# Kernel optimization log

Measured on AMD Instinct MI355X. Metric: run time of the kernel, lower is better.

Reference implementation:

```python
import jax, jax.numpy as jnp
import numpy as np
import math

H = 32          # num heads
D_NOPE = 128
D_ROPE = 64
D_QK = D_NOPE + D_ROPE   # 192
D_V = 128
KV_LORA = 512
EPS = 1e-6
ROPE_THETA = 10000.0
FACTOR = 40.0
BETA_FAST, BETA_SLOW = 32.0, 1.0
ORIG_MAX_POS = 4096
MSCALE_ALL_DIM = 1.0


def _yarn_inv_freq():
    dim = D_ROPE
    pos_freqs = ROPE_THETA ** (np.arange(0, dim, 2, dtype=np.float64) / dim)
    inv_extra = 1.0 / pos_freqs
    inv_inter = 1.0 / (FACTOR * pos_freqs)

    def corr_dim(n_rot):
        return dim * math.log(ORIG_MAX_POS / (n_rot * 2 * math.pi)) / (2 * math.log(ROPE_THETA))
    low = max(math.floor(corr_dim(BETA_FAST)), 0)
    high = min(math.ceil(corr_dim(BETA_SLOW)), dim - 1)
    ramp = np.clip((np.arange(dim // 2, dtype=np.float64) - low) / max(high - low, 1e-3), 0, 1)
    inv_freq_mask = 1.0 - ramp  # extrapolation_factor = 1
    inv_freq = inv_inter * (1 - inv_freq_mask) + inv_extra * inv_freq_mask
    return jnp.asarray(inv_freq, dtype=jnp.float32)  # [D_ROPE//2]


def _apply_rope_gptj(x, cos, sin):
    # x: [T, n, D_ROPE]; cos/sin: [T, D_ROPE//2]; interleaved (is_neox_style=False)
    x2 = x.reshape(*x.shape[:-1], D_ROPE // 2, 2)
    x1, xo = x2[..., 0], x2[..., 1]
    c = cos[:, None, :]
    s = sin[:, None, :]
    r1 = x1 * c - xo * s
    r2 = xo * c + x1 * s
    return jnp.stack([r1, r2], axis=-1).reshape(x.shape)


def _rmsnorm(x, w):
    var = jnp.mean(x.astype(jnp.float32) ** 2, axis=-1, keepdims=True)
    return (x * jax.lax.rsqrt(var + EPS)) * w


def setup_inputs() -> dict:
    key = jax.random.key(0)
    ks = jax.random.split(key, 8)
    T, HID = 2048, 4096
    def w(k, shape, fan_in):
        return jax.random.normal(k, shape, dtype=jnp.float32) * (1.0 / math.sqrt(fan_in))
    return {
        "positions": jnp.arange(T, dtype=jnp.int32),
        "hidden_states": jax.random.normal(ks[0], (T, HID), dtype=jnp.float32),
        "Wqa": w(ks[1], (HID, 1536), HID),
        "q_a_ln": jnp.ones((1536,), dtype=jnp.float32),
        "Wqb": w(ks[2], (1536, H * D_QK), 1536),
        "Wkva": w(ks[3], (HID, KV_LORA + D_ROPE), HID),
        "kv_a_ln": jnp.ones((KV_LORA,), dtype=jnp.float32),
        "Wkvb": w(ks[4], (KV_LORA, H * (D_NOPE + D_V)), KV_LORA),
        "Wo": w(ks[5], (H * D_V, HID), H * D_V),
    }


def reference(positions, hidden_states, Wqa, q_a_ln, Wqb, Wkva, kv_a_ln, Wkvb, Wo):
    T = hidden_states.shape[0]
    # softmax scaling with yarn mscale correction
    mscale = 0.1 * MSCALE_ALL_DIM * math.log(FACTOR) + 1.0
    scaling = (D_QK ** -0.5) * mscale * mscale

    # --- low-rank Q path ---
    q = hidden_states @ Wqa                       # [T, 1536]
    q = _rmsnorm(q, q_a_ln)
    q = (q @ Wqb).reshape(T, H, D_QK)             # [T, H, 192]
    q_nope, q_pe = q[..., :D_NOPE], q[..., D_NOPE:]

    # --- low-rank latent KV path ---
    latent = hidden_states @ Wkva                 # [T, 576]
    kv_a = _rmsnorm(latent[:, :KV_LORA], kv_a_ln) # [T, 512]
    k_pe = latent[:, None, KV_LORA:]              # [T, 1, 64]
    kv = (kv_a @ Wkvb).reshape(T, H, D_NOPE + D_V)
    k_nope = kv[..., :D_NOPE]                     # [T, H, 128]
    v = kv[..., D_NOPE:]                          # [T, H, 128]

    # --- decoupled RoPE on rope slice only ---
    inv_freq = _yarn_inv_freq()
    freqs = positions.astype(jnp.float32)[:, None] * inv_freq[None, :]  # [T, 32]
    cos, sin = jnp.cos(freqs), jnp.sin(freqs)
    q_pe = _apply_rope_gptj(q_pe, cos, sin)       # [T, H, 64]
    k_pe = _apply_rope_gptj(k_pe, cos, sin)       # [T, 1, 64]

    q = jnp.concatenate([q_nope, q_pe], axis=-1)                      # [T, H, 192]
    k = jnp.concatenate([k_nope, jnp.broadcast_to(k_pe, (T, H, D_ROPE))], axis=-1)

    # --- causal MHA over assembled K/V ---
    scores = jnp.einsum('thd,shd->hts', q, k) * scaling               # [H, T, T]
    causal = positions[None, :, None] >= positions[None, None, :]
    scores = jnp.where(causal, scores, jnp.finfo(scores.dtype).min)
    probs = jax.nn.softmax(scores, axis=-1)
    attn = jnp.einsum('hts,shd->thd', probs, v).reshape(T, H * D_V)
    return attn @ Wo                                                   # [T, 4096]
```

## Files before the change

### kernel.cpp

```cpp
#include <hip/hip_runtime.h>
#include <math.h>

typedef __bf16 bf16x8 __attribute__((ext_vector_type(8)));
typedef float f32x4 __attribute__((ext_vector_type(4)));
typedef unsigned short u16;
typedef unsigned int u32;

#define T_SEQ 2048
#define NHEAD 32

__device__ __forceinline__ u16 f2bu(float f){
  u32 u = __float_as_uint(f);
  u32 r = (u + 0x7fffu + ((u >> 16) & 1u)) >> 16;
  return (u16)r;
}

__device__ __forceinline__ void gload_lds16(const void* g, void* l){
  __builtin_amdgcn_global_load_lds((const __attribute__((address_space(1))) u32*)g,
                                   (__attribute__((address_space(3))) u32*)l, 16, 0, 0);
}

__global__ void cast_f32_bf16(const float* __restrict__ in, u16* __restrict__ out, int n4){
  int i = blockIdx.x * blockDim.x + threadIdx.x;
  int stride = gridDim.x * blockDim.x;
  for (; i < n4; i += stride){
    float4 v = ((const float4*)in)[i];
    ushort4 o;
    o.x = f2bu(v.x); o.y = f2bu(v.y); o.z = f2bu(v.z); o.w = f2bu(v.w);
    ((ushort4*)out)[i] = o;
  }
}

__global__ void transpose_cast(const float* __restrict__ src, u16* __restrict__ dst,
                               int K, int N){
  __shared__ float tile[64][65];
  int k0 = blockIdx.x * 64, n0 = blockIdx.y * 64;
  int t = threadIdx.x;
  int rr = t >> 4, c4 = (t & 15) * 4;
  #pragma unroll
  for (int i = 0; i < 4; i++){
    int r = rr + i * 16;
    int n = n0 + c4;
    float4 v;
    if (n < N) v = *(const float4*)(src + (size_t)(k0 + r) * N + n);
    else       v = make_float4(0.f, 0.f, 0.f, 0.f);
    tile[r][c4]     = v.x;
    tile[r][c4 + 1] = v.y;
    tile[r][c4 + 2] = v.z;
    tile[r][c4 + 3] = v.w;
  }
  __syncthreads();
  #pragma unroll
  for (int i = 0; i < 4; i++){
    int n = rr + i * 16;
    ushort4 o;
    o.x = f2bu(tile[c4 + 0][n]);
    o.y = f2bu(tile[c4 + 1][n]);
    o.z = f2bu(tile[c4 + 2][n]);
    o.w = f2bu(tile[c4 + 3][n]);
    *(ushort4*)(dst + (size_t)(n0 + n) * K + k0 + c4) = o;
  }
}

__global__ void rope_table(const int* __restrict__ positions, float* __restrict__ cosT,
                           float* __restrict__ sinT, float lo, float denom){
  int idx = blockIdx.x * blockDim.x + threadIdx.x;
  if (idx >= T_SEQ * 32) return;
  int t = idx >> 5, i = idx & 31;
  float pf = powf(10000.f, (float)i / 32.f);
  float inv_extra = 1.f / pf;
  float inv_inter = 1.f / (40.f * pf);
  float ramp = fminf(fmaxf(((float)i - lo) / denom, 0.f), 1.f);
  float invf = inv_inter * ramp + inv_extra * (1.f - ramp);
  float fr = (float)positions[t] * invf;
  cosT[idx] = cosf(fr);
  sinT[idx] = sinf(fr);
}

__global__ void rmsnorm_cast(const float* __restrict__ in, int istride, int n,
                             const float* __restrict__ w, u16* __restrict__ out, int ostride){
  int row = blockIdx.x;
  const float* x = in + (size_t)row * istride;
  float ss = 0.f;
  for (int c = threadIdx.x; c < n; c += blockDim.x){ float v = x[c]; ss += v * v; }
  #pragma unroll
  for (int off = 1; off < 64; off <<= 1) ss += __shfl_xor(ss, off);
  __shared__ float wsum[4];
  if ((threadIdx.x & 63) == 0) wsum[threadIdx.x >> 6] = ss;
  __syncthreads();
  float tot = wsum[0] + wsum[1] + wsum[2] + wsum[3];
  float scale = rsqrtf(tot / (float)n + 1e-6f);
  for (int c = threadIdx.x; c < n; c += blockDim.x)
    out[(size_t)row * ostride + c] = f2bu(x[c] * scale * w[c]);
}

__global__ void rope_kpe(const float* __restrict__ lat, int lstride, int loff,
                         const float* __restrict__ cosT,
                         const float* __restrict__ sinT, u16* __restrict__ kpe){
  int idx = blockIdx.x * blockDim.x + threadIdx.x;
  if (idx >= T_SEQ * 32) return;
  int t = idx >> 5, i = idx & 31;
  float x1 = lat[(size_t)t * lstride + loff + 2 * i];
  float x2 = lat[(size_t)t * lstride + loff + 2 * i + 1];
  float c = cosT[idx], s = sinT[idx];
  kpe[t * 64 + 2 * i]     = f2bu(x1 * c - x2 * s);
  kpe[t * 64 + 2 * i + 1] = f2bu(x2 * c + x1 * s);
}

__global__ void build_vt(const u16* __restrict__ Vtmp, u16* __restrict__ Vt){
  __shared__ u16 tile[128][72];
  int t0 = blockIdx.x * 64;
  int h = blockIdx.y;
  #pragma unroll
  for (int i = 0; i < 32; i++){
    int lin = threadIdx.x + i * 256;
    int tt = lin >> 7, dd = lin & 127;
    tile[dd][tt] = Vtmp[(size_t)(t0 + tt) * 4096 + h * 128 + dd];
  }
  __syncthreads();
  #pragma unroll
  for (int i = 0; i < 32; i++){
    int lin = threadIdx.x + i * 256;
    int dd = lin >> 6, tt = lin & 63;
    Vt[(size_t)(h * 128 + dd) * T_SEQ + t0 + tt] = tile[dd][tt];
  }
}

template<int EPI>
__global__ __launch_bounds__(256) void gemm_bt(const u16* __restrict__ A, const u16* __restrict__ BT,
                                               float* __restrict__ C, u16* __restrict__ O1,
                                               u16* __restrict__ O2,
                                               const float* __restrict__ cosT,
                                               const float* __restrict__ sinT,
                                               float scaling, int M, int N, int K){
  __shared__ __align__(1024) char lds[32768];
  const int tid = threadIdx.x;
  const int wave = tid >> 6, lane = tid & 63;
  const int lg = lane >> 4, lm = lane & 15;

  int gx = gridDim.x;
  int nwg = gx * gridDim.y;
  int orig = blockIdx.y * gx + blockIdx.x;
  int qq = nwg >> 3, rr_ = nwg & 7, xc = orig & 7, rest = orig >> 3;
  int wg = (xc < rr_ ? xc * (qq + 1) : rr_ * (qq + 1) + (xc - rr_) * qq) + rest;
  const int bn = (wg % gx) * 128, bm = (wg / gx) * 128;

  const int wr = (wave >> 1) * 64, wc = (wave & 1) * 64;
  f32x4 acc[4][4] = {};
  int srow[2], scol[2], soff[2];
  #pragma unroll
  for (int j = 0; j < 2; j++){
    int o = (wave * 2 + j) * 1024 + lane * 16;
    int row = o >> 6;
    int cg = ((o >> 4) & 3) ^ ((row >> 1) & 3);
    srow[j] = row; scol[j] = cg * 8; soff[j] = (wave * 2 + j) * 1024;
  }

  #pragma unroll
  for (int j = 0; j < 2; j++){
    gload_lds16(A  + (size_t)(bm + srow[j]) * K + scol[j], lds + soff[j]);
    gload_lds16(BT + (size_t)(bn + srow[j]) * K + scol[j], lds + 16384 + soff[j]);
  }

  int cur = 0;
  for (int k0 = 0; k0 < K; k0 += 32){
    if (k0 + 32 < K){
      char* dA = lds + (cur ^ 1) * 8192;
      char* dB = lds + 16384 + (cur ^ 1) * 8192;
      #pragma unroll
      for (int j = 0; j < 2; j++){
        gload_lds16(A  + (size_t)(bm + srow[j]) * K + k0 + 32 + scol[j], dA + soff[j]);
        gload_lds16(BT + (size_t)(bn + srow[j]) * K + k0 + 32 + scol[j], dB + soff[j]);
      }
      asm volatile("s_waitcnt vmcnt(4)" ::: "memory");
    } else {
      asm volatile("s_waitcnt vmcnt(0)" ::: "memory");
    }
    __builtin_amdgcn_sched_barrier(0);
    __builtin_amdgcn_s_barrier();

    const char* ldsA = lds + cur * 8192;
    const char* ldsB = lds + 16384 + cur * 8192;
    bf16x8 af[4], bfr[4];
    #pragma unroll
    for (int m = 0; m < 4; m++){
      int r = wr + m * 16 + lm;
      af[m] = *(const bf16x8*)(ldsA + r * 64 + ((lg ^ ((r >> 1) & 3)) << 4));
    }
    #pragma unroll
    for (int n = 0; n < 4; n++){
      int r = wc + n * 16 + lm;
      bfr[n] = *(const bf16x8*)(ldsB + r * 64 + ((lg ^ ((r >> 1) & 3)) << 4));
    }
    __builtin_amdgcn_s_setprio(1);
    #pragma unroll
    for (int m = 0; m < 4; m++)
      #pragma unroll
      for (int n = 0; n < 4; n++)
        acc[m][n] = __builtin_amdgcn_mfma_f32_16x16x32_bf16(af[m], bfr[n], acc[m][n], 0, 0, 0);
    __builtin_amdgcn_s_setprio(0);
    __builtin_amdgcn_s_barrier();
    cur ^= 1;
  }

  #pragma unroll
  for (int m = 0; m < 4; m++)
    #pragma unroll
    for (int n = 0; n < 4; n++)
      #pragma unroll
      for (int q = 0; q < 4; q++){
        int r = bm + wr + m * 16 + lg * 4 + q;
        int c = bn + wc + n * 16 + lm;
        float v = acc[m][n][q];
        if (EPI == 0){
          C[(size_t)r * N + c] = v;
        } else if (EPI == 1){
          float vp = __shfl_xor(v, 1);
          int h = c / 192, d = c - h * 192;
          float outv;
          if (d < 128) outv = v;
          else {
            int i = (d - 128) >> 1;
            float co = cosT[r * 32 + i], si = sinT[r * 32 + i];
            outv = (d & 1) ? (v * co + vp * si) : (v * co - vp * si);
          }
          O1[(size_t)h * T_SEQ * 192 + (size_t)r * 192 + d] = f2bu(outv * scaling);
        } else {
          int h = c >> 8, d = c & 255;
          if (d < 128) O1[(size_t)h * T_SEQ * 128 + (size_t)r * 128 + d] = f2bu(v);
          else         O2[(size_t)r * 4096 + h * 128 + (d - 128)] = f2bu(v);
        }
      }
}

__global__ __launch_bounds__(512, 1) void flash_attn(const u16* __restrict__ Qp, const u16* __restrict__ Kp,
                                                     const u16* __restrict__ kpe, const u16* __restrict__ Vt,
                                                     u16* __restrict__ attnb){
  const int b = blockIdx.x;
  const int h = (b & 7) + 8 * ((b >> 3) & 3);
  const int s = b >> 5;
  const int tid = threadIdx.x;
  const int wave = tid >> 6, lane = tid & 63;
  const int lg = lane >> 4, lm = lane & 15;

  __shared__ __align__(1024) char lds[141312];
  u16* Pw = (u16*)(lds + 122880 + wave * 2304);

  const u16* KpH = Kp + (size_t)h * T_SEQ * 128;
  const u16* VtH = Vt + (size_t)h * 128 * T_SEQ;

  int kO[3], kLoc[3], kPE[3];
  #pragma unroll
  for (int j = 0; j < 3; j++){
    int o = tid + 512 * j;
    int r = o / 24, c = o - r * 24;
    int cx = c ^ (r & 7);
    kO[j] = o * 16;
    if (cx < 16){ kPE[j] = 0; kLoc[j] = r * 128 + cx * 8; }
    else        { kPE[j] = 1; kLoc[j] = r * 64 + (cx - 16) * 8; }
  }
  int vO[2], vSrc[2];
  #pragma unroll
  for (int j = 0; j < 2; j++){
    int o = (tid + 512 * j) * 16;
    int d = o >> 7, c = (o & 127) >> 4;
    vO[j] = o; vSrc[j] = d * T_SEQ + ((c ^ (d & 7)) << 3);
  }

  #define STAGE_KV(t, bi)                                                              \
    do {                                                                               \
      char* _k = lds + (bi) * 24576;                                                   \
      char* _v = lds + 73728 + (bi) * 16384;                                           \
      _Pragma("unroll")                                                                \
      for (int j = 0; j < 3; j++){                                                     \
        const u16* _s = kPE[j] ? (kpe + (size_t)(t) * 4096 + kLoc[j])                  \
                               : (KpH + (size_t)(t) * 8192 + kLoc[j]);                 \
        gload_lds16(_s, _k + kO[j]);                                                   \
      }                                                                                \
      _Pragma("unroll")                                                                \
      for (int j = 0; j < 2; j++) gload_lds16(VtH + vSrc[j] + (t) * 64, _v + vO[j]);   \
    } while (0)

  #pragma unroll 1
  for (int rep = 0; rep < 2; rep++){
    const int qt = rep ? s : (15 - s);
    const int qbase = qt * 128 + wave * 16;
    const int nt = 2 * qt + 2;

    __syncthreads();

    bf16x8 qf[6];
    const u16* Qbase = Qp + (size_t)(h * T_SEQ + qbase + lm) * 192 + lg * 8;
    #pragma unroll
    for (int dk = 0; dk < 6; dk++) qf[dk] = *(const bf16x8*)(Qbase + dk * 32);

    f32x4 o_[8] = {};
    float m_[4], l_[4];
    #pragma unroll
    for (int q = 0; q < 4; q++){ m_[q] = -3.0e38f; l_[q] = 0.f; }

    STAGE_KV(0, 0);
    if (nt > 1) STAGE_KV(1, 1);

    int cur = 0;
    #pragma unroll 1
    for (int kt = 0; kt < nt; kt++){
      const int t0 = kt * 64;
      if (kt < nt - 1) asm volatile("s_waitcnt vmcnt(5)" ::: "memory");
      else             asm volatile("s_waitcnt vmcnt(0)" ::: "memory");
      __builtin_amdgcn_sched_barrier(0);
      __builtin_amdgcn_s_barrier();
      if (kt + 2 < nt){
        int nb = cur + 2; if (nb >= 3) nb -= 3;
        STAGE_KV(kt + 2, nb);
      }
      const char* Kb = lds + cur * 24576;
      const char* Vb = lds + 73728 + cur * 16384;

      f32x4 s_[4] = {};
      __builtin_amdgcn_s_setprio(1);
      #pragma unroll
      for (int hh = 0; hh < 4; hh++){
        const int r = hh * 16 + lm;
        const int rb = r * 384, rx = r & 7;
        #pragma unroll
        for (int dk = 0; dk < 6; dk++){
          bf16x8 kf = *(const bf16x8*)(Kb + rb + (((dk * 4 + lg) ^ rx) << 4));
          s_[hh] = __builtin_amdgcn_mfma_f32_16x16x32_bf16(qf[dk], kf, s_[hh], 0, 0, 0);
        }
      }
      __builtin_amdgcn_s_setprio(0);
      #pragma unroll
      for (int hh = 0; hh < 4; hh++)
        #pragma unroll
        for (int q = 0; q < 4; q++){
          int col = t0 + hh * 16 + lm;
          int qrow = qbase + lg * 4 + q;
          if (col > qrow) s_[hh][q] = -3.0e38f;
        }
      float pm[4];
      #pragma unroll
      for (int q = 0; q < 4; q++)
        pm[q] = fmaxf(fmaxf(s_[0][q], s_[1][q]), fmaxf(s_[2][q], s_[3][q]));
      int ok = (pm[0] <= m_[0] + 8.f) & (pm[1] <= m_[1] + 8.f) &
               (pm[2] <= m_[2] + 8.f) & (pm[3] <= m_[3] + 8.f);
      if (!__all(ok)){
        #pragma unroll
        for (int q = 0; q < 4; q++){
          float v = pm[q];
          #pragma unroll
          for (int off = 8; off; off >>= 1) v = fmaxf(v, __shfl_xor(v, off));
          float mn = fmaxf(m_[q], v);
          float alpha = (m_[q] <= -1.0e37f) ? 0.f : __expf(m_[q] - mn);
          l_[q] *= alpha;
          #pragma unroll
          for (int n = 0; n < 8; n++) o_[n][q] *= alpha;
          m_[q] = mn;
        }
      }
      #pragma unroll
      for (int q = 0; q < 4; q++){
        #pragma unroll
        for (int hh = 0; hh < 4; hh++){
          float p = __expf(s_[hh][q] - m_[q]);
          l_[q] += p;
          Pw[(lg * 4 + q) * 72 + hh * 16 + lm] = f2bu(p);
        }
      }
      asm volatile("s_waitcnt lgkmcnt(0)" ::: "memory");
      __builtin_amdgcn_sched_barrier(0);
      __builtin_amdgcn_s_setprio(1);
      #pragma unroll
      for (int ks = 0; ks < 2; ks++){
        bf16x8 pf = *(const bf16x8*)((const char*)Pw + lm * 144 + ks * 64 + lg * 16);
        #pragma unroll
        for (int n = 0; n < 8; n++){
          const int d = n * 16 + lm;
          bf16x8 vf = *(const bf16x8*)(Vb + d * 128 + (((ks * 4 + lg) ^ (d & 7)) << 4));
          o_[n] = __builtin_amdgcn_mfma_f32_16x16x32_bf16(pf, vf, o_[n], 0, 0, 0);
        }
      }
      __builtin_amdgcn_s_setprio(0);
      cur = (cur == 2) ? 0 : cur + 1;
    }

    #pragma unroll
    for (int q = 0; q < 4; q++){
      #pragma unroll
      for (int off = 8; off; off >>= 1) l_[q] += __shfl_xor(l_[q], off);
    }
    float inv[4];
    #pragma unroll
    for (int q = 0; q < 4; q++) inv[q] = 1.f / l_[q];
    #pragma unroll
    for (int n = 0; n < 8; n++)
      #pragma unroll
      for (int q = 0; q < 4; q++){
        int r = qbase + lg * 4 + q;
        attnb[(size_t)r * 4096 + h * 128 + n * 16 + lm] = f2bu(o_[n][q] * inv[q]);
      }
  }
  #undef STAGE_KV
}

extern "C" void kernel_launch(void* const* d_in, const int* in_sizes, int n_in,
                              void* d_out, int out_size, void* d_ws, size_t ws_size,
                              hipStream_t stream){
  const int*   positions = (const int*)d_in[0];
  const float* hidden    = (const float*)d_in[1];
  const float* Wqa       = (const float*)d_in[2];
  const float* q_a_ln    = (const float*)d_in[3];
  const float* Wqb       = (const float*)d_in[4];
  const float* Wkva      = (const float*)d_in[5];
  const float* kv_a_ln   = (const float*)d_in[6];
  const float* Wkvb      = (const float*)d_in[7];
  const float* Wo        = (const float*)d_in[8];
  float* out = (float*)d_out;
  char* ws = (char*)d_ws;

  const size_t o_hid  = 0;
  const size_t o_cos  = 16777216;
  const size_t o_sin  = 17039360;
  const size_t o_kpe  = 17301504;
  const size_t o_comb = 17563648;
  const size_t o_qln  = 35389440;
  const size_t o_kva  = 41680896;
  const size_t o_W    = 43778048;
  const size_t o_Qp   = 77332480;
  const size_t o_Kp   = 102498304;
  const size_t o_Vtmp = 119275520;
  const size_t o_Vt   = 136052736;
  const size_t o_att  = 152829952;

  u16*   hidB = (u16*)(ws + o_hid);
  float* cosT = (float*)(ws + o_cos);
  float* sinT = (float*)(ws + o_sin);
  u16*   kpe  = (u16*)(ws + o_kpe);
  float* comb = (float*)(ws + o_comb);
  u16*   qln  = (u16*)(ws + o_qln);
  u16*   kva  = (u16*)(ws + o_kva);
  u16*   Wt   = (u16*)(ws + o_W);
  u16*   Qp   = (u16*)(ws + o_Qp);
  u16*   Kp   = (u16*)(ws + o_Kp);
  u16*   Vtmp = (u16*)(ws + o_Vtmp);
  u16*   Vt   = (u16*)(ws + o_Vt);
  u16*   attnb= (u16*)(ws + o_att);

  double mscale = 0.1 * log(40.0) + 1.0;
  float scaling = (float)(pow(192.0, -0.5) * mscale * mscale);
  const double PI = 3.14159265358979323846;
  double cd_fast = 64.0 * log(4096.0 / (32.0 * 2.0 * PI)) / (2.0 * log(10000.0));
  double cd_slow = 64.0 * log(4096.0 / ( 1.0 * 2.0 * PI)) / (2.0 * log(10000.0));
  double lo_d = fmax(floor(cd_fast), 0.0);
  double hi_d = fmin(ceil(cd_slow), 63.0);
  float lo = (float)lo_d;
  float denom = (float)fmax(hi_d - lo_d, 0.001);

  cast_f32_bf16<<<2048, 256, 0, stream>>>(hidden, hidB, T_SEQ * 4096 / 4);
  rope_table<<<256, 256, 0, stream>>>(positions, cosT, sinT, lo, denom);
  transpose_cast<<<dim3(4096 / 64, 1536 / 64), 256, 0, stream>>>(Wqa, Wt, 4096, 1536);
  transpose_cast<<<dim3(4096 / 64, 640 / 64), 256, 0, stream>>>(Wkva, Wt + (size_t)1536 * 4096, 4096, 576);
  gemm_bt<0><<<dim3(2176 / 128, 2048 / 128), 256, 0, stream>>>(hidB, Wt, comb, nullptr, nullptr,
                                                               nullptr, nullptr, 0.f, 2048, 2176, 4096);
  rmsnorm_cast<<<2048, 256, 0, stream>>>(comb, 2176, 1536, q_a_ln, qln, 1536);
  rmsnorm_cast<<<2048, 256, 0, stream>>>(comb + 1536, 2176, 512, kv_a_ln, kva, 512);
  rope_kpe<<<256, 256, 0, stream>>>(comb, 2176, 2048, cosT, sinT, kpe);
  transpose_cast<<<dim3(1536 / 64, 6144 / 64), 256, 0, stream>>>(Wqb, Wt, 1536, 6144);
  gemm_bt<1><<<dim3(6144 / 128, 2048 / 128), 256, 0, stream>>>(qln, Wt, nullptr, Qp, nullptr,
                                                               cosT, sinT, scaling, 2048, 6144, 1536);
  transpose_cast<<<dim3(512 / 64, 8192 / 64), 256, 0, stream>>>(Wkvb, Wt, 512, 8192);
  gemm_bt<2><<<dim3(8192 / 128, 2048 / 128), 256, 0, stream>>>(kva, Wt, nullptr, Kp, Vtmp,
                                                               nullptr, nullptr, 0.f, 2048, 8192, 512);
  build_vt<<<dim3(T_SEQ / 64, NHEAD), 256, 0, stream>>>(Vtmp, Vt);
  flash_attn<<<256, 512, 0, stream>>>(Qp, Kp, kpe, Vt, attnb);
  transpose_cast<<<dim3(4096 / 64, 4096 / 64), 256, 0, stream>>>(Wo, Wt, 4096, 4096);
  gemm_bt<0><<<dim3(4096 / 128, 2048 / 128), 256, 0, stream>>>(attnb, Wt, out, nullptr, nullptr,
                                                               nullptr, nullptr, 0.f, 2048, 4096, 4096);
}
```

Before: 412.6 us.

## Split attention into one q-tile per block with smaller KV tiles; batch weight transposes

The flash attention kernel now gives each block a single 128-row query tile and launches 512 blocks instead of 256 blocks that each processed a paired light and heavy tile. KV tiles shrink from 64 to 32 keys, roughly halving LDS use, and the launch bound asks for up to 4 blocks per CU so more blocks can be resident at once. The aim is better CU occupancy and latency hiding, at the cost of losing the causal load-balance pairing, more loop iterations and barriers, and possible register pressure or spills from the tighter launch bound. Separately, the five weight transpose/cast launches are merged into one batched kernel writing to distinct buffers. The attention output now reuses the hidden-state bf16 buffer, which is no longer needed after the first GEMM.

```diff
diff --git a/kernel.cpp b/kernel.cpp
--- a/kernel.cpp
+++ b/kernel.cpp
@@ -31,10 +31,9 @@
   }
 }
 
-__global__ void transpose_cast(const float* __restrict__ src, u16* __restrict__ dst,
-                               int K, int N){
+__device__ __forceinline__ void tc_body(const float* __restrict__ src, u16* __restrict__ dst,
+                                        int K, int N, int k0, int n0){
   __shared__ float tile[64][65];
-  int k0 = blockIdx.x * 64, n0 = blockIdx.y * 64;
   int t = threadIdx.x;
   int rr = t >> 4, c4 = (t & 15) * 4;
   #pragma unroll
@@ -60,6 +59,22 @@
     o.w = f2bu(tile[c4 + 3][n]);
     *(ushort4*)(dst + (size_t)(n0 + n) * K + k0 + c4) = o;
   }
+}
+
+__global__ __launch_bounds__(256) void transpose_batch(
+    const float* __restrict__ Wqa, u16* __restrict__ WqaT,
+    const float* __restrict__ Wkva, u16* __restrict__ WkvaT,
+    const float* __restrict__ Wqb, u16* __restrict__ WqbT,
+    const float* __restrict__ Wkvb, u16* __restrict__ WkvbT,
+    const float* __restrict__ Wo, u16* __restrict__ WoT){
+  int bid = blockIdx.x;
+  const float* s; u16* d; int K, N, gx, l;
+  if (bid < 1536)      { s = Wqa;  d = WqaT;  K = 4096; N = 1536; gx = 64; l = bid; }
+  else if (bid < 2176) { s = Wkva; d = WkvaT; K = 4096; N = 576;  gx = 64; l = bid - 1536; }
+  else if (bid < 4480) { s = Wqb;  d = WqbT;  K = 1536; N = 6144; gx = 24; l = bid - 2176; }
+  else if (bid < 5504) { s = Wkvb; d = WkvbT; K = 512;  N = 8192; gx = 8;  l = bid - 4480; }
+  else                 { s = Wo;   d = WoT;   K = 4096; N = 4096; gx = 64; l = bid - 5504; }
+  tc_body(s, d, K, N, (l % gx) * 64, (l / gx) * 64);
 }
 
 __global__ void rope_table(const int* __restrict__ positions, float* __restrict__ cosT,
@@ -233,173 +248,158 @@
       }
 }
 
-__global__ __launch_bounds__(512, 1) void flash_attn(const u16* __restrict__ Qp, const u16* __restrict__ Kp,
+__global__ __launch_bounds__(512, 4) void flash_attn(const u16* __restrict__ Qp, const u16* __restrict__ Kp,
                                                      const u16* __restrict__ kpe, const u16* __restrict__ Vt,
                                                      u16* __restrict__ attnb){
   const int b = blockIdx.x;
   const int h = (b & 7) + 8 * ((b >> 3) & 3);
-  const int s = b >> 5;
+  const int qt = 15 - (b >> 5);
   const int tid = threadIdx.x;
   const int wave = tid >> 6, lane = tid & 63;
   const int lg = lane >> 4, lm = lane & 15;
-
-  __shared__ __align__(1024) char lds[141312];
-  u16* Pw = (u16*)(lds + 122880 + wave * 2304);
+  const int qbase = qt * 128 + wave * 16;
+
+  __shared__ __align__(1024) char lds[71680];
+  u16* Pw = (u16*)(lds + 61440 + wave * 1280);
 
   const u16* KpH = Kp + (size_t)h * T_SEQ * 128;
   const u16* VtH = Vt + (size_t)h * 128 * T_SEQ;
 
-  int kO[3], kLoc[3], kPE[3];
-  #pragma unroll
-  for (int j = 0; j < 3; j++){
+  int kO[2], kLoc[2], kPE[2];
+  #pragma unroll
+  for (int j = 0; j < 2; j++){
     int o = tid + 512 * j;
-    int r = o / 24, c = o - r * 24;
+    int r = (o / 24) & 31, c = o % 24;
     int cx = c ^ (r & 7);
     kO[j] = o * 16;
     if (cx < 16){ kPE[j] = 0; kLoc[j] = r * 128 + cx * 8; }
     else        { kPE[j] = 1; kLoc[j] = r * 64 + (cx - 16) * 8; }
   }
-  int vO[2], vSrc[2];
-  #pragma unroll
-  for (int j = 0; j < 2; j++){
-    int o = (tid + 512 * j) * 16;
-    int d = o >> 7, c = (o & 127) >> 4;
-    vO[j] = o; vSrc[j] = d * T_SEQ + ((c ^ (d & 7)) << 3);
-  }
+  int vO, vSrc;
+  { int o = tid; int d = o >> 2, c = o & 3; vO = o * 16; vSrc = d * T_SEQ + ((c ^ (d & 3)) << 3); }
 
   #define STAGE_KV(t, bi)                                                              \
     do {                                                                               \
-      char* _k = lds + (bi) * 24576;                                                   \
-      char* _v = lds + 73728 + (bi) * 16384;                                           \
-      _Pragma("unroll")                                                                \
-      for (int j = 0; j < 3; j++){                                                     \
-        const u16* _s = kPE[j] ? (kpe + (size_t)(t) * 4096 + kLoc[j])                  \
-                               : (KpH + (size_t)(t) * 8192 + kLoc[j]);                 \
-        gload_lds16(_s, _k + kO[j]);                                                   \
-      }                                                                                \
-      _Pragma("unroll")                                                                \
-      for (int j = 0; j < 2; j++) gload_lds16(VtH + vSrc[j] + (t) * 64, _v + vO[j]);   \
+      char* _k = lds + (bi) * 12288;                                                   \
+      char* _v = lds + 36864 + (bi) * 8192;                                            \
+      { const u16* _s = kPE[0] ? (kpe + (size_t)(t) * 2048 + kLoc[0])                  \
+                               : (KpH + (size_t)(t) * 4096 + kLoc[0]);                 \
+        gload_lds16(_s, _k + kO[0]); }                                                 \
+      if (tid < 256){                                                                  \
+        const u16* _s = kPE[1] ? (kpe + (size_t)(t) * 2048 + kLoc[1])                  \
+                               : (KpH + (size_t)(t) * 4096 + kLoc[1]);                 \
+        gload_lds16(_s, _k + kO[1]); }                                                 \
+      gload_lds16(VtH + vSrc + (t) * 32, _v + vO);                                     \
     } while (0)
 
+  const int nt = 4 * qt + 4;
+
+  bf16x8 qf[6];
+  const u16* Qbase = Qp + (size_t)(h * T_SEQ + qbase + lm) * 192 + lg * 8;
+  #pragma unroll
+  for (int dk = 0; dk < 6; dk++) qf[dk] = *(const bf16x8*)(Qbase + dk * 32);
+
+  f32x4 o_[8] = {};
+  float m_[4], l_[4];
+  #pragma unroll
+  for (int q = 0; q < 4; q++){ m_[q] = -3.0e38f; l_[q] = 0.f; }
+
+  STAGE_KV(0, 0);
+  STAGE_KV(1, 1);
+
+  int cur = 0;
   #pragma unroll 1
-  for (int rep = 0; rep < 2; rep++){
-    const int qt = rep ? s : (15 - s);
-    const int qbase = qt * 128 + wave * 16;
-    const int nt = 2 * qt + 2;
-
-    __syncthreads();
-
-    bf16x8 qf[6];
-    const u16* Qbase = Qp + (size_t)(h * T_SEQ + qbase + lm) * 192 + lg * 8;
-    #pragma unroll
-    for (int dk = 0; dk < 6; dk++) qf[dk] = *(const bf16x8*)(Qbase + dk * 32);
-
-    f32x4 o_[8] = {};
-    float m_[4], l_[4];
-    #pragma unroll
-    for (int q = 0; q < 4; q++){ m_[q] = -3.0e38f; l_[q] = 0.f; }
-
-    STAGE_KV(0, 0);
-    if (nt > 1) STAGE_KV(1, 1);
-
-    int cur = 0;
-    #pragma unroll 1
-    for (int kt = 0; kt < nt; kt++){
-      const int t0 = kt * 64;
-      if (kt < nt - 1) asm volatile("s_waitcnt vmcnt(5)" ::: "memory");
-      else             asm volatile("s_waitcnt vmcnt(0)" ::: "memory");
-      __builtin_amdgcn_sched_barrier(0);
-      __builtin_amdgcn_s_barrier();
-      if (kt + 2 < nt){
-        int nb = cur + 2; if (nb >= 3) nb -= 3;
-        STAGE_KV(kt + 2, nb);
-      }
-      const char* Kb = lds + cur * 24576;
-      const char* Vb = lds + 73728 + cur * 16384;
-
-      f32x4 s_[4] = {};
-      __builtin_amdgcn_s_setprio(1);
-      #pragma unroll
-      for (int hh = 0; hh < 4; hh++){
-        const int r = hh * 16 + lm;
-        const int rb = r * 384, rx = r & 7;
+  for (int kt = 0; kt < nt; kt++){
+    const int t0 = kt * 32;
+    if (kt < nt - 1) asm volatile("s_waitcnt vmcnt(2)" ::: "memory");
+    else             asm volatile("s_waitcnt vmcnt(0)" ::: "memory");
+    __builtin_amdgcn_sched_barrier(0);
+    __builtin_amdgcn_s_barrier();
+    if (kt + 2 < nt){
+      int nb = cur + 2; if (nb >= 3) nb -= 3;
+      STAGE_KV(kt + 2, nb);
+    }
+    const char* Kb = lds + cur * 12288;
+    const char* Vb = lds + 36864 + cur * 8192;
+
+    f32x4 s_[2] = {};
+    __builtin_amdgcn_s_setprio(1);
+    #pragma unroll
+    for (int hh = 0; hh < 2; hh++){
+      const int r = hh * 16 + lm;
+      const int rb = r * 384, rx = r & 7;
+      #pragma unroll
+      for (int dk = 0; dk < 6; dk++){
+        bf16x8 kf = *(const bf16x8*)(Kb + rb + (((dk * 4 + lg) ^ rx) << 4));
+        s_[hh] = __builtin_amdgcn_mfma_f32_16x16x32_bf16(qf[dk], kf, s_[hh], 0, 0, 0);
+      }
+    }
+    __builtin_amdgcn_s_setprio(0);
+    #pragma unroll
+    for (int hh = 0; hh < 2; hh++)
+      #pragma unroll
+      for (int q = 0; q < 4; q++){
+        int col = t0 + hh * 16 + lm;
+        int qrow = qbase + lg * 4 + q;
+        if (col > qrow) s_[hh][q] = -3.0e38f;
+      }
+    float pm[4];
+    #pragma unroll
+    for (int q = 0; q < 4; q++) pm[q] = fmaxf(s_[0][q], s_[1][q]);
+    int ok = (pm[0] <= m_[0] + 8.f) & (pm[1] <= m_[1] + 8.f) &
+             (pm[2] <= m_[2] + 8.f) & (pm[3] <= m_[3] + 8.f);
+    if (!__all(ok)){
+      #pragma unroll
+      for (int q = 0; q < 4; q++){
+        float v = pm[q];
         #pragma unroll
-        for (int dk = 0; dk < 6; dk++){
-          bf16x8 kf = *(const bf16x8*)(Kb + rb + (((dk * 4 + lg) ^ rx) << 4));
-          s_[hh] = __builtin_amdgcn_mfma_f32_16x16x32_bf16(qf[dk], kf, s_[hh], 0, 0, 0);
-        }
-      }
-      __builtin_amdgcn_s_setprio(0);
-      #pragma unroll
-      for (int hh = 0; hh < 4; hh++)
+        for (int off = 8; off; off >>= 1) v = fmaxf(v, __shfl_xor(v, off));
+        float mn = fmaxf(m_[q], v);
+        float alpha = (m_[q] <= -1.0e37f) ? 0.f : __expf(m_[q] - mn);
+        l_[q] *= alpha;
         #pragma unroll
-        for (int q = 0; q < 4; q++){
-          int col = t0 + hh * 16 + lm;
-          int qrow = qbase + lg * 4 + q;
-          if (col > qrow) s_[hh][q] = -3.0e38f;
-        }
-      float pm[4];
-      #pragma unroll
-      for (int q = 0; q < 4; q++)
-        pm[q] = fmaxf(fmaxf(s_[0][q], s_[1][q]), fmaxf(s_[2][q], s_[3][q]));
-      int ok = (pm[0] <= m_[0] + 8.f) & (pm[1] <= m_[1] + 8.f) &
-               (pm[2] <= m_[2] + 8.f) & (pm[3] <= m_[3] + 8.f);
-      if (!__all(ok)){
-        #pragma unroll
-        for (int q = 0; q < 4; q++){
-          float v = pm[q];
-          #pragma unroll
-          for (int off = 8; off; off >>= 1) v = fmaxf(v, __shfl_xor(v, off));
-          float mn = fmaxf(m_[q], v);
-          float alpha = (m_[q] <= -1.0e37f) ? 0.f : __expf(m_[q] - mn);
-          l_[q] *= alpha;
-          #pragma unroll
-          for (int n = 0; n < 8; n++) o_[n][q] *= alpha;
-          m_[q] = mn;
-        }
-      }
-      #pragma unroll
-      for (int q = 0; q < 4; q++){
-        #pragma unroll
-        for (int hh = 0; hh < 4; hh++){
-          float p = __expf(s_[hh][q] - m_[q]);
-          l_[q] += p;
-          Pw[(lg * 4 + q) * 72 + hh * 16 + lm] = f2bu(p);
-        }
-      }
-      asm volatile("s_waitcnt lgkmcnt(0)" ::: "memory");
-      __builtin_amdgcn_sched_barrier(0);
-      __builtin_amdgcn_s_setprio(1);
-      #pragma unroll
-      for (int ks = 0; ks < 2; ks++){
-        bf16x8 pf = *(const bf16x8*)((const char*)Pw + lm * 144 + ks * 64 + lg * 16);
-        #pragma unroll
-        for (int n = 0; n < 8; n++){
-          const int d = n * 16 + lm;
-          bf16x8 vf = *(const bf16x8*)(Vb + d * 128 + (((ks * 4 + lg) ^ (d & 7)) << 4));
-          o_[n] = __builtin_amdgcn_mfma_f32_16x16x32_bf16(pf, vf, o_[n], 0, 0, 0);
-        }
-      }
-      __builtin_amdgcn_s_setprio(0);
-      cur = (cur == 2) ? 0 : cur + 1;
-    }
-
+        for (int n = 0; n < 8; n++) o_[n][q] *= alpha;
+        m_[q] = mn;
+      }
+    }
     #pragma unroll
     for (int q = 0; q < 4; q++){
       #pragma unroll
-      for (int off = 8; off; off >>= 1) l_[q] += __shfl_xor(l_[q], off);
-    }
-    float inv[4];
-    #pragma unroll
-    for (int q = 0; q < 4; q++) inv[q] = 1.f / l_[q];
-    #pragma unroll
-    for (int n = 0; n < 8; n++)
-      #pragma unroll
-      for (int q = 0; q < 4; q++){
-        int r = qbase + lg * 4 + q;
-        attnb[(size_t)r * 4096 + h * 128 + n * 16 + lm] = f2bu(o_[n][q] * inv[q]);
-      }
-  }
+      for (int hh = 0; hh < 2; hh++){
+        float p = __expf(s_[hh][q] - m_[q]);
+        l_[q] += p;
+        Pw[(lg * 4 + q) * 40 + hh * 16 + lm] = f2bu(p);
+      }
+    }
+    asm volatile("s_waitcnt lgkmcnt(0)" ::: "memory");
+    __builtin_amdgcn_sched_barrier(0);
+    bf16x8 pf = *(const bf16x8*)((const char*)Pw + lm * 80 + lg * 16);
+    __builtin_amdgcn_s_setprio(1);
+    #pragma unroll
+    for (int n = 0; n < 8; n++){
+      const int d = n * 16 + lm;
+      bf16x8 vf = *(const bf16x8*)(Vb + d * 64 + ((lg ^ (d & 3)) << 4));
+      o_[n] = __builtin_amdgcn_mfma_f32_16x16x32_bf16(pf, vf, o_[n], 0, 0, 0);
+    }
+    __builtin_amdgcn_s_setprio(0);
+    cur = (cur == 2) ? 0 : cur + 1;
+  }
+
+  #pragma unroll
+  for (int q = 0; q < 4; q++){
+    #pragma unroll
+    for (int off = 8; off; off >>= 1) l_[q] += __shfl_xor(l_[q], off);
+  }
+  float inv[4];
+  #pragma unroll
+  for (int q = 0; q < 4; q++) inv[q] = 1.f / l_[q];
+  #pragma unroll
+  for (int n = 0; n < 8; n++)
+    #pragma unroll
+    for (int q = 0; q < 4; q++){
+      int r = qbase + lg * 4 + q;
+      attnb[(size_t)r * 4096 + h * 128 + n * 16 + lm] = f2bu(o_[n][q] * inv[q]);
+    }
   #undef STAGE_KV
 }
 
@@ -418,33 +418,40 @@
   float* out = (float*)d_out;
   char* ws = (char*)d_ws;
 
-  const size_t o_hid  = 0;
-  const size_t o_cos  = 16777216;
-  const size_t o_sin  = 17039360;
-  const size_t o_kpe  = 17301504;
-  const size_t o_comb = 17563648;
-  const size_t o_qln  = 35389440;
-  const size_t o_kva  = 41680896;
-  const size_t o_W    = 43778048;
-  const size_t o_Qp   = 77332480;
-  const size_t o_Kp   = 102498304;
-  const size_t o_Vtmp = 119275520;
-  const size_t o_Vt   = 136052736;
-  const size_t o_att  = 152829952;
-
-  u16*   hidB = (u16*)(ws + o_hid);
-  float* cosT = (float*)(ws + o_cos);
-  float* sinT = (float*)(ws + o_sin);
-  u16*   kpe  = (u16*)(ws + o_kpe);
-  float* comb = (float*)(ws + o_comb);
-  u16*   qln  = (u16*)(ws + o_qln);
-  u16*   kva  = (u16*)(ws + o_kva);
-  u16*   Wt   = (u16*)(ws + o_W);
-  u16*   Qp   = (u16*)(ws + o_Qp);
-  u16*   Kp   = (u16*)(ws + o_Kp);
-  u16*   Vtmp = (u16*)(ws + o_Vtmp);
-  u16*   Vt   = (u16*)(ws + o_Vt);
-  u16*   attnb= (u16*)(ws + o_att);
+  const size_t o_hidB  = 0;
+  const size_t o_cos   = 16777216;
+  const size_t o_sin   = 17039360;
+  const size_t o_kpe   = 17301504;
+  const size_t o_comb  = 17563648;
+  const size_t o_qln   = 35389440;
+  const size_t o_kva   = 41680896;
+  const size_t o_WqaT  = 43778048;
+  const size_t o_WkvaT = 56360960;
+  const size_t o_WqbT  = 61603840;
+  const size_t o_WkvbT = 80478208;
+  const size_t o_Qp    = 88866816;
+  const size_t o_Kp    = 114032640;
+  const size_t o_Vtmp  = 130809856;
+  const size_t o_Vt    = 147587072;
+  const size_t o_WoT   = 164364288;
+
+  u16*   hidB  = (u16*)(ws + o_hidB);
+  u16*   attnb = (u16*)(ws + o_hidB);
+  float* cosT  = (float*)(ws + o_cos);
+  float* sinT  = (float*)(ws + o_sin);
+  u16*   kpe   = (u16*)(ws + o_kpe);
+  float* comb  = (float*)(ws + o_comb);
+  u16*   qln   = (u16*)(ws + o_qln);
+  u16*   kva   = (u16*)(ws + o_kva);
+  u16*   WqaT  = (u16*)(ws + o_WqaT);
+  u16*   WkvaT = (u16*)(ws + o_WkvaT);
+  u16*   WqbT  = (u16*)(ws + o_WqbT);
+  u16*   WkvbT = (u16*)(ws + o_WkvbT);
+  u16*   Qp    = (u16*)(ws + o_Qp);
+  u16*   Kp    = (u16*)(ws + o_Kp);
+  u16*   Vtmp  = (u16*)(ws + o_Vtmp);
+  u16*   Vt    = (u16*)(ws + o_Vt);
+  u16*   WoT   = (u16*)(ws + o_WoT);
 
   double mscale = 0.1 * log(40.0) + 1.0;
   float scaling = (float)(pow(192.0, -0.5) * mscale * mscale);
@@ -456,24 +463,21 @@
   float lo = (float)lo_d;
   float denom = (float)fmax(hi_d - lo_d, 0.001);
 
+  transpose_batch<<<9600, 256, 0, stream>>>(Wqa, WqaT, Wkva, WkvaT, Wqb, WqbT,
+                                            Wkvb, WkvbT, Wo, WoT);
   cast_f32_bf16<<<2048, 256, 0, stream>>>(hidden, hidB, T_SEQ * 4096 / 4);
   rope_table<<<256, 256, 0, stream>>>(positions, cosT, sinT, lo, denom);
-  transpose_cast<<<dim3(4096 / 64, 1536 / 64), 256, 0, stream>>>(Wqa, Wt, 4096, 1536);
-  transpose_cast<<<dim3(4096 / 64, 640 / 64), 256, 0, stream>>>(Wkva, Wt + (size_t)1536 * 4096, 4096, 576);
-  gemm_bt<0><<<dim3(2176 / 128, 2048 / 128), 256, 0, stream>>>(hidB, Wt, comb, nullptr, nullptr,
+  gemm_bt<0><<<dim3(2176 / 128, 2048 / 128), 256, 0, stream>>>(hidB, WqaT, comb, nullptr, nullptr,
                                                                nullptr, nullptr, 0.f, 2048, 2176, 4096);
   rmsnorm_cast<<<2048, 256, 0, stream>>>(comb, 2176, 1536, q_a_ln, qln, 1536);
   rmsnorm_cast<<<2048, 256, 0, stream>>>(comb + 1536, 2176, 512, kv_a_ln, kva, 512);
   rope_kpe<<<256, 256, 0, stream>>>(comb, 2176, 2048, cosT, sinT, kpe);
-  transpose_cast<<<dim3(1536 / 64, 6144 / 64), 256, 0, stream>>>(Wqb, Wt, 1536, 6144);
-  gemm_bt<1><<<dim3(6144 / 128, 2048 / 128), 256, 0, stream>>>(qln, Wt, nullptr, Qp, nullptr,
+  gemm_bt<1><<<dim3(6144 / 128, 2048 / 128), 256, 0, stream>>>(qln, WqbT, nullptr, Qp, nullptr,
                                                                cosT, sinT, scaling, 2048, 6144, 1536);
-  transpose_cast<<<dim3(512 / 64, 8192 / 64), 256, 0, stream>>>(Wkvb, Wt, 512, 8192);
-  gemm_bt<2><<<dim3(8192 / 128, 2048 / 128), 256, 0, stream>>>(kva, Wt, nullptr, Kp, Vtmp,
+  gemm_bt<2><<<dim3(8192 / 128, 2048 / 128), 256, 0, stream>>>(kva, WkvbT, nullptr, Kp, Vtmp,
                                                                nullptr, nullptr, 0.f, 2048, 8192, 512);
   build_vt<<<dim3(T_SEQ / 64, NHEAD), 256, 0, stream>>>(Vtmp, Vt);
-  flash_attn<<<256, 512, 0, stream>>>(Qp, Kp, kpe, Vt, attnb);
-  transpose_cast<<<dim3(4096 / 64, 4096 / 64), 256, 0, stream>>>(Wo, Wt, 4096, 4096);
-  gemm_bt<0><<<dim3(4096 / 128, 2048 / 128), 256, 0, stream>>>(attnb, Wt, out, nullptr, nullptr,
+  flash_attn<<<512, 512, 0, stream>>>(Qp, Kp, kpe, Vt, attnb);
+  gemm_bt<0><<<dim3(4096 / 128, 2048 / 128), 256, 0, stream>>>(attnb, WoT, out, nullptr, nullptr,
                                                                nullptr, nullptr, 0.f, 2048, 4096, 4096);
 }
```

New measurement: 412.2 us. About the same (-0.1%).
